# Kernel optimization log

Measured on AMD Instinct MI355X. Metric: run time of the kernel, lower is better.

## Reference

```python
import jax, jax.numpy as jnp
import numpy as np

# Static layer configuration (from init_kwargs)
C_IN, H, W = 8, 32, 32
C_OUT, KH, KW = 16, 3, 3
SH, SW = 1, 1
PH, PW = 1, 1
OH = (H + 2 * PH - KH) // SH + 1
OW = (W + 2 * PW - KW) // SW + 1
N_IN = C_IN * H * W      # 8192 input-layer neurons
N_OUT = C_OUT * OH * OW  # 16384 output-layer neurons


def setup_inputs() -> dict:
    key = jax.random.key(0)
    k1, k2, k3, k4 = jax.random.split(key, 4)
    base = jax.random.normal(k1, (C_IN, H, W), dtype=jnp.float32)
    rad = jax.random.uniform(k2, (C_IN, H, W), dtype=jnp.float32)
    return {
        "concrete_lower": base - rad,   # ensure lower <= upper
        "concrete_upper": base + rad,
        "weights": jax.random.normal(k3, (C_OUT, C_IN, KH, KW), dtype=jnp.float32) * 0.1,
        "bias": jax.random.normal(k4, (C_OUT,), dtype=jnp.float32) * 0.1,
    }


def build_abstract_matrix(weights, bias):
    """Vectorized equivalent of _create_conv2d_channel_v0 over all channels.

    Produces M of shape (N_IN+1, N_OUT+1): column (c*OH*OW + i*OW + j) holds the
    affine coefficients (over flattened input neurons, bias in last row) of
    output pixel (c, i, j); last column is the homogeneous [0...0, 1] column.
    """
    idy = jnp.arange(OH)[:, None] * SH - PH + jnp.arange(KH)[None, :]  # (OH, KH)
    idx = jnp.arange(OW)[:, None] * SW - PW + jnp.arange(KW)[None, :]  # (OW, KW)
    valid = (((idy >= 0) & (idy < H))[:, :, None, None]
             & ((idx >= 0) & (idx < W))[None, None, :, :])             # (OH, KH, OW, KW)

    cin = jnp.arange(C_IN)
    # broadcast layout: (C_OUT, C_IN, OH, KH, OW, KW)
    rows = (cin[None, :, None, None, None, None] * (H * W)
            + idy[None, None, :, :, None, None] * W
            + idx[None, None, None, None, :, :])
    oc = jnp.arange(C_OUT)
    cols = (oc[:, None, None, None, None, None] * (OH * OW)
            + jnp.arange(OH)[None, None, :, None, None, None] * OW
            + jnp.arange(OW)[None, None, None, None, :, None])
    vals = weights[:, :, None, :, None, :]  # (C_OUT, C_IN, 1, KH, 1, KW)

    shape = (C_OUT, C_IN, OH, KH, OW, KW)
    rows_b = jnp.broadcast_to(rows, shape).reshape(-1)
    cols_b = jnp.broadcast_to(cols, shape).reshape(-1)
    vals_b = jnp.broadcast_to(vals, shape).reshape(-1)
    valid_b = jnp.broadcast_to(valid[None, None], shape).reshape(-1)
    # padding taps (out of input bounds) -> out-of-range row index, dropped by scatter
    rows_b = jnp.where(valid_b, rows_b, N_IN + 1)

    M = jnp.zeros((N_IN + 1, N_OUT + 1), dtype=jnp.float32)
    M = M.at[rows_b, cols_b].set(vals_b, mode="drop")
    M = M.at[N_IN, :N_OUT].set(jnp.repeat(bias, OH * OW))  # bias row per output pixel
    M = M.at[N_IN, N_OUT].set(1.0)                          # homogeneous corner
    return M


def back_substitute(M, l_in, u_in, lower=True):
    # Interval evaluation of the affine map: positive coeffs pair with one bound,
    # negative with the other; last row of M is the bias.
    Wc = M[:-1, :]
    b = M[-1, :]
    pos = jnp.maximum(Wc, 0.0)
    neg = jnp.minimum(Wc, 0.0)
    if lower:
        return l_in @ pos + u_in @ neg + b
    return u_in @ pos + l_in @ neg + b


def reference(concrete_lower, concrete_upper, weights, bias):
    M = build_abstract_matrix(weights, bias)  # abstract lower == upper for a conv layer
    l = concrete_lower.reshape(-1)
    u = concrete_upper.reshape(-1)
    lo = back_substitute(M, l, u, lower=True)[:N_OUT].reshape(C_OUT, OH, OW)
    hi = back_substitute(M, l, u, lower=False)[:N_OUT].reshape(C_OUT, OH, OW)
    return (lo, hi, M)
```

## Files before the change

### kernel.cpp

```cpp
#include <hip/hip_runtime.h>

#define C_IN  8
#define H     32
#define W     32
#define C_OUT 16
#define KH    3
#define KW    3
#define OH    32
#define OW    32
#define N_IN  (C_IN * H * W)
#define N_OUT (C_OUT * OH * OW)
#define MROWS (N_IN + 1)
#define MCOLS (N_OUT + 1)

#define N_BOUND_BLOCKS 64
#define N_FLAT_BLOCKS  2048
#define N_FULL_ITER 64
#define TAIL_BLKS   8
#define STEP_ELEMS  (N_FLAT_BLOCKS * 1024)
#define STEP_ROW    127
#define STEP_COL    16257

typedef float v4f __attribute__((ext_vector_type(4)));

__global__ __launch_bounds__(256, 8) void fused_kernel(const float* __restrict__ l_in,
                                                       const float* __restrict__ u_in,
                                                       const float* __restrict__ wts,
                                                       const float* __restrict__ bias,
                                                       float* __restrict__ out,
                                                       float* __restrict__ M) {
    const int b = blockIdx.x;
    const int t = threadIdx.x;

    if (b < N_FLAT_BLOCKS) {
        __shared__ float ldsW[C_OUT * C_IN * 9];
        for (int s = t; s < C_OUT * C_IN * 9; s += 256) ldsW[s] = wts[s];
        __syncthreads();

        const int E0 = b << 10;
        int r  = E0 >> 14;
        int c0 = (E0 & 16383) - r;
        if (c0 < 0) { c0 += MCOLS; r -= 1; }

        const int t4 = 4 * t;
        float* dst = M + (size_t)E0 + t4;
        const v4f zero = {0.0f, 0.0f, 0.0f, 0.0f};

        for (int n = 0; n < N_FULL_ITER + 1; ++n) {
            if (n == N_FULL_ITER && b >= TAIL_BLKS) break;

            int colt = c0 + t4;
            int rt   = r;
            if (colt >= MCOLS) { colt -= MCOLS; rt = r + 1; }

            const int iy = (rt >> 5) & 31;
            const int ix = rt & 31;
            const int j0 = colt & 31;
            const int i0 = (colt >> 5) & 31;

            const bool edge = (colt + 3 >= 16384);
            const bool jh   = (((ix - j0 + 1) & 31) <= 5);
            const bool ih   = (((iy - i0 + 1) & 31) <= 3);

            if (edge | (jh & ih)) {
                float vv[4];
                #pragma unroll
                for (int q = 0; q < 4; ++q) {
                    int  cq    = colt + q;
                    bool carry = (cq >= MCOLS);
                    int  cq2   = carry ? cq - MCOLS : cq;
                    int  rq    = rt + (carry ? 1 : 0);
                    int  cin   = rq >> 10;
                    int  iyq   = (rq >> 5) & 31;
                    int  ixq   = rq & 31;
                    int  c     = cq2 >> 10;
                    int  i     = (cq2 >> 5) & 31;
                    int  j     = cq2 & 31;
                    int  kh    = iyq + 1 - i;
                    int  kw    = ixq + 1 - j;
                    bool ok    = ((unsigned)kh < 3u) & ((unsigned)kw < 3u) & (cq2 < N_OUT);
                    int  idx   = ok ? (c * 72 + cin * 9 + kh * 3 + kw) : 0;
                    float w    = ldsW[idx];
                    vv[q]      = ok ? w : 0.0f;
                }
                v4f v4 = {vv[0], vv[1], vv[2], vv[3]};
                *(v4f*)dst = v4;
            } else {
                *(v4f*)dst = zero;
            }

            dst += (size_t)STEP_ELEMS;
            c0  += STEP_COL;
            r   += STEP_ROW;
            if (c0 >= MCOLS) { c0 -= MCOLS; r += 1; }
        }
        return;
    }

    if (b == N_FLAT_BLOCKS) {
        float* __restrict__ Mrow = M + (size_t)N_IN * MCOLS;
        #pragma unroll
        for (int k = 0; k < 16; ++k) {
            float bv = bias[k];
            v4f v = {bv, bv, bv, bv};
            *(v4f*)(Mrow + (k << 10) + 4 * t) = v;
        }
        if (t == 0) Mrow[N_OUT] = 1.0f;
        return;
    }

    int tid = (b - (N_FLAT_BLOCKS + 1)) * 256 + t;
    int c = tid >> 10;
    int i = (tid >> 5) & 31;
    int j = tid & 31;

    float lo = bias[c];
    float hi = lo;

    #pragma unroll
    for (int cin = 0; cin < C_IN; ++cin) {
        #pragma unroll
        for (int kh = 0; kh < KH; ++kh) {
            int iy = i - 1 + kh;
            if ((unsigned)iy >= (unsigned)H) continue;
            #pragma unroll
            for (int kw = 0; kw < KW; ++kw) {
                int ix = j - 1 + kw;
                if ((unsigned)ix >= (unsigned)W) continue;
                float w = wts[c * 72 + cin * 9 + kh * 3 + kw];
                int   r = cin * 1024 + iy * 32 + ix;
                float a  = w * l_in[r];
                float bb = w * u_in[r];
                lo += fminf(a, bb);
                hi += fmaxf(a, bb);
            }
        }
    }
    out[tid]         = lo;
    out[N_OUT + tid] = hi;
}

extern "C" void kernel_launch(void* const* d_in, const int* in_sizes, int n_in,
                              void* d_out, int out_size, void* d_ws, size_t ws_size,
                              hipStream_t stream) {
    const float* lower = (const float*)d_in[0];
    const float* upper = (const float*)d_in[1];
    const float* wts   = (const float*)d_in[2];
    const float* bias  = (const float*)d_in[3];

    float* out = (float*)d_out;
    float* M   = out + 2 * N_OUT;

    const int grid = N_FLAT_BLOCKS + 1 + N_BOUND_BLOCKS;
    hipLaunchKernelGGL(fused_kernel, dim3(grid), dim3(256), 0, stream,
                       lower, upper, wts, bias, out, M);
}
```

Baseline: 544.0 us.

## Zero M with hipMemsetAsync and scatter only nonzero conv weights

Drops the fused kernel that wrote every element of the dense 8193x16385 matrix, including zeros, with computed masks. M is now cleared with hipMemsetAsync, and a scatter kernel writes only the 144 possibly nonzero entries per input row, with the bias row and the bounds computation following in the same launch. The aim is to let the driver's fill path handle the bulk zeroing and cut per-element index arithmetic. The cost is an extra operation on the stream, plus scattered 4-byte writes that partially overwrite cache lines the memset just wrote.

```diff
diff --git a/kernel.cpp b/kernel.cpp
--- a/kernel.cpp
+++ b/kernel.cpp
@@ -13,103 +13,57 @@
 #define MROWS (N_IN + 1)
 #define MCOLS (N_OUT + 1)
 
-#define N_BOUND_BLOCKS 64
-#define N_FLAT_BLOCKS  2048
-#define N_FULL_ITER 64
-#define TAIL_BLKS   8
-#define STEP_ELEMS  (N_FLAT_BLOCKS * 1024)
-#define STEP_ROW    127
-#define STEP_COL    16257
-
 typedef float v4f __attribute__((ext_vector_type(4)));
 
-__global__ __launch_bounds__(256, 8) void fused_kernel(const float* __restrict__ l_in,
-                                                       const float* __restrict__ u_in,
-                                                       const float* __restrict__ wts,
-                                                       const float* __restrict__ bias,
-                                                       float* __restrict__ out,
-                                                       float* __restrict__ M) {
+#define NB_SCATTER 4608
+#define NB_BIAS    16
+#define NB_BOUNDS  64
+
+__global__ __launch_bounds__(256) void scatter_kernel(const float* __restrict__ l_in,
+                                                      const float* __restrict__ u_in,
+                                                      const float* __restrict__ wts,
+                                                      const float* __restrict__ bias,
+                                                      float* __restrict__ out,
+                                                      float* __restrict__ M) {
     const int b = blockIdx.x;
     const int t = threadIdx.x;
 
-    if (b < N_FLAT_BLOCKS) {
-        __shared__ float ldsW[C_OUT * C_IN * 9];
-        for (int s = t; s < C_OUT * C_IN * 9; s += 256) ldsW[s] = wts[s];
-        __syncthreads();
+    if (b < NB_SCATTER) {
+        const int tid = (b << 8) + t;
+        const int r   = tid / 144;
+        const int k   = tid - r * 144;
+        const int oc  = k / 9;
+        const int q   = k - oc * 9;
+        const int di  = q / 3;
+        const int dj  = q - di * 3;
 
-        const int E0 = b << 10;
-        int r  = E0 >> 14;
-        int c0 = (E0 & 16383) - r;
-        if (c0 < 0) { c0 += MCOLS; r -= 1; }
+        const int cin = r >> 10;
+        const int iy  = (r >> 5) & 31;
+        const int ix  = r & 31;
 
-        const int t4 = 4 * t;
-        float* dst = M + (size_t)E0 + t4;
-        const v4f zero = {0.0f, 0.0f, 0.0f, 0.0f};
+        const int i = iy - 1 + di;
+        const int j = ix - 1 + dj;
 
-        for (int n = 0; n < N_FULL_ITER + 1; ++n) {
-            if (n == N_FULL_ITER && b >= TAIL_BLKS) break;
-
-            int colt = c0 + t4;
-            int rt   = r;
-            if (colt >= MCOLS) { colt -= MCOLS; rt = r + 1; }
-
-            const int iy = (rt >> 5) & 31;
-            const int ix = rt & 31;
-            const int j0 = colt & 31;
-            const int i0 = (colt >> 5) & 31;
-
-            const bool edge = (colt + 3 >= 16384);
-            const bool jh   = (((ix - j0 + 1) & 31) <= 5);
-            const bool ih   = (((iy - i0 + 1) & 31) <= 3);
-
-            if (edge | (jh & ih)) {
-                float vv[4];
-                #pragma unroll
-                for (int q = 0; q < 4; ++q) {
-                    int  cq    = colt + q;
-                    bool carry = (cq >= MCOLS);
-                    int  cq2   = carry ? cq - MCOLS : cq;
-                    int  rq    = rt + (carry ? 1 : 0);
-                    int  cin   = rq >> 10;
-                    int  iyq   = (rq >> 5) & 31;
-                    int  ixq   = rq & 31;
-                    int  c     = cq2 >> 10;
-                    int  i     = (cq2 >> 5) & 31;
-                    int  j     = cq2 & 31;
-                    int  kh    = iyq + 1 - i;
-                    int  kw    = ixq + 1 - j;
-                    bool ok    = ((unsigned)kh < 3u) & ((unsigned)kw < 3u) & (cq2 < N_OUT);
-                    int  idx   = ok ? (c * 72 + cin * 9 + kh * 3 + kw) : 0;
-                    float w    = ldsW[idx];
-                    vv[q]      = ok ? w : 0.0f;
-                }
-                v4f v4 = {vv[0], vv[1], vv[2], vv[3]};
-                *(v4f*)dst = v4;
-            } else {
-                *(v4f*)dst = zero;
-            }
-
-            dst += (size_t)STEP_ELEMS;
-            c0  += STEP_COL;
-            r   += STEP_ROW;
-            if (c0 >= MCOLS) { c0 -= MCOLS; r += 1; }
+        if (((unsigned)i < 32u) & ((unsigned)j < 32u)) {
+            const int kh = 2 - di;
+            const int kw = 2 - dj;
+            const float w = wts[oc * 72 + cin * 9 + kh * 3 + kw];
+            M[(size_t)r * MCOLS + (oc << 10) + (i << 5) + j] = w;
         }
         return;
     }
 
-    if (b == N_FLAT_BLOCKS) {
+    if (b < NB_SCATTER + NB_BIAS) {
+        const int bb = b - NB_SCATTER;
         float* __restrict__ Mrow = M + (size_t)N_IN * MCOLS;
-        #pragma unroll
-        for (int k = 0; k < 16; ++k) {
-            float bv = bias[k];
-            v4f v = {bv, bv, bv, bv};
-            *(v4f*)(Mrow + (k << 10) + 4 * t) = v;
-        }
-        if (t == 0) Mrow[N_OUT] = 1.0f;
+        const float bv = bias[bb];
+        v4f v = {bv, bv, bv, bv};
+        *(v4f*)(Mrow + (bb << 10) + 4 * t) = v;
+        if (bb == 0 && t == 0) Mrow[N_OUT] = 1.0f;
         return;
     }
 
-    int tid = (b - (N_FLAT_BLOCKS + 1)) * 256 + t;
+    int tid = (b - (NB_SCATTER + NB_BIAS)) * 256 + t;
     int c = tid >> 10;
     int i = (tid >> 5) & 31;
     int j = tid & 31;
@@ -151,7 +105,9 @@
     float* out = (float*)d_out;
     float* M   = out + 2 * N_OUT;
 
-    const int grid = N_FLAT_BLOCKS + 1 + N_BOUND_BLOCKS;
-    hipLaunchKernelGGL(fused_kernel, dim3(grid), dim3(256), 0, stream,
+    hipMemsetAsync(M, 0, (size_t)MROWS * MCOLS * sizeof(float), stream);
+
+    const int grid = NB_SCATTER + NB_BIAS + NB_BOUNDS;
+    hipLaunchKernelGGL(scatter_kernel, dim3(grid), dim3(256), 0, stream,
                        lower, upper, wts, bias, out, M);
 }
```

Measured after the change: 579.9 us. +6.6%, slower.
